# Performance work log

Measured on AMD Instinct MI355X. Metric: run time of the kernel, lower is better.

Reference implementation:

```python
import jax, jax.numpy as jnp
import numpy as np

B, L, D = 4, 8192, 1024
H, HD = 16, 64  # num_heads, head_dim (qkv_features = H*HD = 1024)
EPS = 1e-06


def elu_feature_map(x):
    return jax.nn.elu(x) + 1.0


def setup_inputs() -> dict:
    key = jax.random.key(0)
    ks = jax.random.split(key, 9)
    # xavier-uniform-ish scales
    def xav(k, shape, fan_in, fan_out):
        lim = jnp.sqrt(6.0 / (fan_in + fan_out))
        return jax.random.uniform(k, shape, jnp.float32, -lim, lim)
    x = jax.random.normal(ks[0], (B, L, D), jnp.float32)
    Wq = xav(ks[1], (D, H, HD), D, H * HD)
    Wk = xav(ks[2], (D, H, HD), D, H * HD)
    Wv = xav(ks[3], (D, H, HD), D, H * HD)
    Wo = xav(ks[4], (H, HD, D), H * HD, D)
    bq = jax.random.normal(ks[5], (H, HD), jnp.float32) * 1e-06
    bk = jax.random.normal(ks[6], (H, HD), jnp.float32) * 1e-06
    bv = jax.random.normal(ks[7], (H, HD), jnp.float32) * 1e-06
    bo = jax.random.normal(ks[8], (D,), jnp.float32) * 1e-06
    return {"x": x, "Wq": Wq, "bq": bq, "Wk": Wk, "bk": bk,
            "Wv": Wv, "bv": bv, "Wo": Wo, "bo": bo}


def reference(x, Wq, bq, Wk, bk, Wv, bv, Wo, bo):
    # QKV projections (DenseGeneral axis=-1 -> (H, HD))
    q = jnp.einsum('nld,dhk->nlhk', x, Wq) + bq  # [B,L,H,HD]
    k = jnp.einsum('nld,dhk->nlhk', x, Wk) + bk
    v = jnp.einsum('nld,dhk->nlhk', x, Wv) + bv
    # Kernelized linear attention
    qf = elu_feature_map(q)
    kf = elu_feature_map(k)
    kv = jnp.einsum('nshd,nshm->nhmd', kf, v)          # [B,H,HD,HD]
    z = 1.0 / (jnp.einsum('nlhd,nhd->nlh', qf, jnp.sum(kf, axis=1)) + EPS)
    y = jnp.einsum('nlhd,nhmd,nlh->nlhm', qf, kv, z)   # [B,L,H,HD]
    # Output projection (DenseGeneral over (-2,-1))
    out = jnp.einsum('nlhm,hmd->nld', y, Wo) + bo      # [B,L,D]
    return out
```

## Files before the change

### kernel.cpp

```cpp
#include <hip/hip_runtime.h>
#include <stdint.h>

typedef unsigned short u16;
typedef __attribute__((ext_vector_type(8))) short bf16x8;
typedef __attribute__((ext_vector_type(8))) unsigned short u16x8;
typedef __attribute__((ext_vector_type(4))) unsigned short u16x4;
typedef __attribute__((ext_vector_type(4))) float f32x4;

#define AS1 __attribute__((address_space(1)))
#define AS3 __attribute__((address_space(3)))

__device__ __forceinline__ u16 f32_to_bf16(float f) {
  unsigned int u = __builtin_bit_cast(unsigned int, f);
  u += 0x7FFFu + ((u >> 16) & 1u);
  return (u16)(u >> 16);
}
__device__ __forceinline__ float bf16_to_f32(u16 s) {
  return __builtin_bit_cast(float, (unsigned int)s << 16);
}
__device__ __forceinline__ void g2lds16(const void* g, void* l) {
  __builtin_amdgcn_global_load_lds((const AS1 void*)g, (AS3 void*)l, 16, 0, 0);
}

__global__ __launch_bounds__(256) void cvt_x(const float* __restrict__ x, u16* __restrict__ xb) {
  size_t base = ((size_t)blockIdx.x * 256 + threadIdx.x) * 8;
  const size_t stride = (size_t)2048 * 256 * 8;
  #pragma unroll
  for (int it = 0; it < 8; ++it, base += stride) {
    float4 a = *(const float4*)(x + base);
    float4 b = *(const float4*)(x + base + 4);
    u16x8 o;
    o[0]=f32_to_bf16(a.x); o[1]=f32_to_bf16(a.y); o[2]=f32_to_bf16(a.z); o[3]=f32_to_bf16(a.w);
    o[4]=f32_to_bf16(b.x); o[5]=f32_to_bf16(b.y); o[6]=f32_to_bf16(b.z); o[7]=f32_to_bf16(b.w);
    *(u16x8*)(xb + base) = o;
  }
}

__global__ void cvt_wt(const float* __restrict__ Wq, const float* __restrict__ Wk,
                       const float* __restrict__ Wv, const float* __restrict__ Wo,
                       u16* __restrict__ WT) {
  __shared__ float tile[32][33];
  const float* W = blockIdx.z==0 ? Wq : blockIdx.z==1 ? Wk : blockIdx.z==2 ? Wv : Wo;
  int n0 = blockIdx.x*32, k0 = blockIdx.y*32;
  int tx = threadIdx.x, ty = threadIdx.y;
  for (int r = ty; r < 32; r += 8)
    tile[r][tx] = W[(size_t)(k0+r)*1024 + n0 + tx];
  __syncthreads();
  u16* out = WT + (size_t)blockIdx.z*1024*1024;
  for (int r = ty; r < 32; r += 8)
    out[(size_t)(n0+r)*1024 + k0 + tx] = f32_to_bf16(tile[tx][r]);
}

__global__ __launch_bounds__(256) void init_vvT(u16* __restrict__ vvT) {
  int idx = blockIdx.x*256 + threadIdx.x;
  int p = idx >> 14, rem = idx & 16383;
  int row = 64 + (rem >> 10), col8 = (rem & 1023) * 8;
  u16 v = (row == 64) ? (u16)0x3F80 : (u16)0;
  u16x8 o = {v,v,v,v,v,v,v,v};
  *(u16x8*)(vvT + ((size_t)p*80 + row)*8192 + col8) = o;
}

template<int MODE>
__global__ __launch_bounds__(512) void gemm8(const u16* __restrict__ A, const u16* __restrict__ WT,
    const float* __restrict__ bq, const float* __restrict__ bk, const float* __restrict__ bv,
    u16* __restrict__ qf, u16* __restrict__ kfT, u16* __restrict__ vvT,
    float* __restrict__ fout) {
  extern __shared__ u16 lds[];
  const int z = (MODE==0) ? blockIdx.y : 3;
  const u16* Bt = WT + (size_t)z*1048576;
  int bid = blockIdx.x;
  int swz = (bid & 7)*64 + (bid >> 3);
  int rb = swz >> 2, cb = swz & 3;
  const int gm0 = rb*256, gn0 = cb*256;
  const int t = threadIdx.x, w = t>>6, l = t&63;
  const int wm = w>>2, wn = w&3;
  const int lrow = l & 15, lks = l >> 4;
  const int csw = (l&7) ^ (l>>3);
  const u16* aBase = A  + (size_t)(gm0 + w*8 + (l>>3))*1024 + csw*8;
  const u16* bBase = Bt + (size_t)(gn0 + w*8 + (l>>3))*1024 + csw*8;

  f32x4 acc[2][2][4][2];
  const f32x4 vzero = {0.f,0.f,0.f,0.f};
  #pragma unroll
  for (int a0=0;a0<2;++a0)
    #pragma unroll
    for (int b0i=0;b0i<2;++b0i)
      #pragma unroll
      for (int c0=0;c0<4;++c0)
        #pragma unroll
        for (int d0=0;d0<2;++d0) acc[a0][b0i][c0][d0] = vzero;

  #pragma unroll
  for (int half=0; half<2; ++half)
    #pragma unroll
    for (int j=0;j<2;++j) {
      g2lds16(aBase + (half*128 + j*64)*1024, (char*)lds + half*16384 + j*8192 + w*1024);
      g2lds16(bBase + (half*128 + j*64)*1024, (char*)lds + 65536 + half*16384 + j*8192 + w*1024);
    }
  asm volatile("s_waitcnt vmcnt(0)" ::: "memory");
  __builtin_amdgcn_s_barrier();
  asm volatile("" ::: "memory");

  for (int kt = 0; kt < 16; ++kt) {
    const int buf = kt & 1;
    const char* Ab = (const char*)lds + buf*32768;
    const char* Bb = (const char*)lds + 65536 + buf*32768;
    char* An = (char*)lds + (buf^1)*32768;
    char* Bn = (char*)lds + 65536 + (buf^1)*32768;
    const u16* aSrc = aBase + (size_t)(kt+1)*64;
    const u16* bSrc = bBase + (size_t)(kt+1)*64;
    const bool pf = (kt < 15);

    bf16x8 af0[4][2], af1[4][2];
    bf16x8 b0[2][2], b1[2][2];

    #define LD_A(DST,MH)                                                     \
      _Pragma("unroll")                                                      \
      for (int mi=0;mi<4;++mi) {                                             \
        int row = (MH)*128 + wm*64 + mi*16 + lrow;                           \
        _Pragma("unroll")                                                    \
        for (int kx=0;kx<2;++kx)                                             \
          DST[mi][kx] = *(const bf16x8*)(Ab + row*128 + (((kx*4+lks) ^ (row&7))<<4)); \
      }
    #define LD_B(DST,NH)                                                     \
      _Pragma("unroll")                                                      \
      for (int ni=0;ni<2;++ni) {                                             \
        int row = (NH)*128 + wn*32 + ni*16 + lrow;                           \
        _Pragma("unroll")                                                    \
        for (int kx=0;kx<2;++kx)                                             \
          DST[ni][kx] = *(const bf16x8*)(Bb + row*128 + (((kx*4+lks) ^ (row&7))<<4)); \
      }
    #define MFMA16(MH,NH,AF,BF)                                              \
      __builtin_amdgcn_s_setprio(1);                                         \
      _Pragma("unroll")                                                      \
      for (int mi=0;mi<4;++mi)                                               \
        _Pragma("unroll")                                                    \
        for (int ni=0;ni<2;++ni) {                                           \
          acc[MH][NH][mi][ni] = __builtin_amdgcn_mfma_f32_16x16x32_bf16(AF[mi][0], BF[ni][0], acc[MH][NH][mi][ni], 0,0,0); \
          acc[MH][NH][mi][ni] = __builtin_amdgcn_mfma_f32_16x16x32_bf16(AF[mi][1], BF[ni][1], acc[MH][NH][mi][ni], 0,0,0); \
        }                                                                    \
      __builtin_amdgcn_s_setprio(0);                                         \
      __builtin_amdgcn_s_barrier();                                          \
      asm volatile("" ::: "memory");

    LD_A(af0, 0); LD_B(b0, 0);
    if (pf) { g2lds16(aSrc, An + w*1024); g2lds16(aSrc + 64*1024, An + 8192 + w*1024); }
    if (pf) { asm volatile("s_waitcnt vmcnt(4)" ::: "memory"); }
    else    { asm volatile("s_waitcnt vmcnt(2)" ::: "memory"); }
    __builtin_amdgcn_s_barrier();
    asm volatile("" ::: "memory");
    LD_B(b1, 1);
    MFMA16(0, 0, af0, b0);

    if (pf) { g2lds16(bSrc, Bn + w*1024); g2lds16(bSrc + 64*1024, Bn + 8192 + w*1024); }
    if (pf) { asm volatile("s_waitcnt vmcnt(4)" ::: "memory"); }
    else    { asm volatile("s_waitcnt vmcnt(0)" ::: "memory"); }
    __builtin_amdgcn_s_barrier();
    asm volatile("" ::: "memory");
    LD_A(af1, 1);
    MFMA16(0, 1, af0, b1);

    if (pf) { g2lds16(bSrc + 128*1024, Bn + 16384 + w*1024); g2lds16(bSrc + 192*1024, Bn + 24576 + w*1024); }
    __builtin_amdgcn_s_barrier();
    asm volatile("" ::: "memory");
    MFMA16(1, 1, af1, b1);

    if (pf) { g2lds16(aSrc + 128*1024, An + 16384 + w*1024); g2lds16(aSrc + 192*1024, An + 24576 + w*1024); }
    if (pf) { asm volatile("s_waitcnt vmcnt(4)" ::: "memory"); }
    __builtin_amdgcn_s_barrier();
    asm volatile("" ::: "memory");
    MFMA16(1, 0, af1, b0);

    #undef LD_A
    #undef LD_B
    #undef MFMA16
  }

  if (MODE == 0) {
    const float* bias = z==0 ? bq : (z==1 ? bk : bv);
    const bool feat = (z < 2);
    if (z == 0) {
      #pragma unroll
      for (int mh=0;mh<2;++mh)
        #pragma unroll
        for (int nh=0;nh<2;++nh)
          #pragma unroll
          for (int mi=0;mi<4;++mi)
            #pragma unroll
            for (int ni=0;ni<2;++ni) {
              int n = gn0 + nh*128 + wn*32 + ni*16 + lrow;
              float bn = bias[n];
              int h = n>>6, hd = n&63;
              int mbase = gm0 + mh*128 + wm*64 + mi*16 + (lks<<2);
              #pragma unroll
              for (int r=0;r<4;++r) {
                int m = mbase + r;
                float val = acc[mh][nh][mi][ni][r] + bn;
                val = val>0.f ? val+1.f : __expf(val);
                qf[((size_t)((m>>13)*16 + h)*8192 + (m&8191))*64 + hd] = f32_to_bf16(val);
              }
            }
    } else {
      u16* outp = (z==1) ? kfT : vvT;
      const size_t prow = (z==1) ? 64 : 80;
      #pragma unroll
      for (int mh=0;mh<2;++mh)
        #pragma unroll
        for (int nh=0;nh<2;++nh)
          #pragma unroll
          for (int mi=0;mi<4;++mi)
            #pragma unroll
            for (int ni=0;ni<2;++ni) {
              int n = gn0 + nh*128 + wn*32 + ni*16 + lrow;
              float bn = bias[n];
              int h = n>>6, hd = n&63;
              int mbase = gm0 + mh*128 + wm*64 + mi*16 + (lks<<2);
              int b_ = mbase >> 13, s = mbase & 8191;
              u16x4 pk;
              #pragma unroll
              for (int r=0;r<4;++r) {
                float val = acc[mh][nh][mi][ni][r] + bn;
                if (feat) val = val>0.f ? val+1.f : __expf(val);
                pk[r] = f32_to_bf16(val);
              }
              *(u16x4*)(outp + ((size_t)(b_*16 + h)*prow + hd)*8192 + s) = pk;
            }
    }
  } else {
    #pragma unroll
    for (int mh=0;mh<2;++mh)
      #pragma unroll
      for (int nh=0;nh<2;++nh)
        #pragma unroll
        for (int mi=0;mi<4;++mi)
          #pragma unroll
          for (int ni=0;ni<2;++ni) {
            int n = gn0 + nh*128 + wn*32 + ni*16 + lrow;
            float bn = bq[n];
            int mbase = gm0 + mh*128 + wm*64 + mi*16 + (lks<<2);
            #pragma unroll
            for (int r=0;r<4;++r) {
              int m = mbase + r;
              fout[(size_t)m*1024 + n] = acc[mh][nh][mi][ni][r] + bn;
            }
          }
  }
}

__global__ __launch_bounds__(256) void kv_mfma(const u16* __restrict__ kfT, const u16* __restrict__ vvT,
                                               float* __restrict__ pkv) {
  __shared__ __align__(16) u16 lA[80*256];
  __shared__ __align__(16) u16 lB[64*256];
  const int p = blockIdx.x, c = blockIdx.y;
  const int t = threadIdx.x, w = t>>6, l = t&63;
  const int srow = t >> 5;
  const int csw = (t&31) ^ ((t>>5)&7);
  const u16* aRow = vvT + ((size_t)p*80 + srow)*8192 + (size_t)c*512 + csw*8;
  const u16* bRow = kfT + ((size_t)p*64 + srow)*8192 + (size_t)c*512 + csw*8;

  f32x4 acc5[5];
  const f32x4 vzero = {0.f,0.f,0.f,0.f};
  #pragma unroll
  for (int mi=0;mi<5;++mi) acc5[mi] = vzero;

  for (int sub = 0; sub < 2; ++sub) {
    const size_t so = (size_t)sub*256;
    #pragma unroll
    for (int i=0;i<10;++i)
      g2lds16(aRow + (size_t)i*8*8192 + so, (char*)lA + i*4096 + t*16);
    #pragma unroll
    for (int i=0;i<8;++i)
      g2lds16(bRow + (size_t)i*8*8192 + so, (char*)lB + i*4096 + t*16);
    asm volatile("s_waitcnt vmcnt(0)" ::: "memory");
    __builtin_amdgcn_s_barrier();
    asm volatile("" ::: "memory");
    #pragma unroll
    for (int ks=0;ks<8;++ks) {
      const int brow = w*16 + (l&15);
      const int slot = ks*4 + (l>>4);
      bf16x8 bfr = *(const bf16x8*)((const char*)lB + brow*512 + ((slot ^ (brow&7))<<4));
      #pragma unroll
      for (int mi=0;mi<5;++mi) {
        const int arow = mi*16 + (l&15);
        bf16x8 afr = *(const bf16x8*)((const char*)lA + arow*512 + ((slot ^ (arow&7))<<4));
        acc5[mi] = __builtin_amdgcn_mfma_f32_16x16x32_bf16(afr, bfr, acc5[mi], 0,0,0);
      }
    }
    __builtin_amdgcn_s_barrier();
    asm volatile("" ::: "memory");
  }

  float* po = pkv + ((size_t)p*16 + c)*5120;
  #pragma unroll
  for (int mi=0;mi<5;++mi)
    #pragma unroll
    for (int r=0;r<4;++r)
      po[(mi*16 + (l>>4)*4 + r)*64 + w*16 + (l&15)] = acc5[mi][r];
}

__global__ __launch_bounds__(256) void kv_reduce(const float* __restrict__ pkv, u16* __restrict__ bkv) {
  int p = blockIdx.x, t = threadIdx.x;
  for (int i = t; i < 5120; i += 256) {
    float s = 0.f;
    for (int c = 0; c < 16; ++c) s += pkv[((size_t)p*16 + c)*5120 + i];
    bkv[(size_t)p*5120 + i] = f32_to_bf16(s);
  }
}

__global__ __launch_bounds__(256) void y_gemm(const u16* __restrict__ qf, const u16* __restrict__ bkv,
                                              u16* __restrict__ y) {
  __shared__ __align__(16) u16 As[256*64];
  __shared__ __align__(16) u16 Bs[80*64];
  int p = blockIdx.x, rb = blockIdx.y;
  int t = threadIdx.x, wave = t >> 6, lane = t & 63;
  const u16* aslab = qf + ((size_t)p*8192 + (size_t)rb*256)*64;
  for (int i = t*8; i < 5120; i += 2048)
    *(int4*)&Bs[i] = *(const int4*)&bkv[(size_t)p*5120 + i];
  #pragma unroll
  for (int it = 0; it < 8; ++it)
    g2lds16(aslab + it*2048 + t*8, (char*)As + it*4096 + wave*1024);
  __syncthreads();
  const f32x4 vzero = {0.f,0.f,0.f,0.f};
  f32x4 acc[4][5];
  #pragma unroll
  for (int mi=0;mi<4;++mi)
    #pragma unroll
    for (int ni=0;ni<5;++ni) acc[mi][ni] = vzero;
  #pragma unroll
  for (int kk = 0; kk < 64; kk += 32) {
    bf16x8 af[4], bfr[5];
    #pragma unroll
    for (int mi=0;mi<4;++mi)
      af[mi] = *(const bf16x8*)&As[(wave*64 + mi*16 + (lane&15))*64 + kk + (lane>>4)*8];
    #pragma unroll
    for (int ni=0;ni<5;++ni)
      bfr[ni] = *(const bf16x8*)&Bs[(ni*16 + (lane&15))*64 + kk + (lane>>4)*8];
    #pragma unroll
    for (int mi=0;mi<4;++mi)
      #pragma unroll
      for (int ni=0;ni<5;++ni)
        acc[mi][ni] = __builtin_amdgcn_mfma_f32_16x16x32_bf16(af[mi], bfr[ni], acc[mi][ni], 0, 0, 0);
  }
  int b_ = p >> 4, h = p & 15;
  #pragma unroll
  for (int mi=0;mi<4;++mi) {
    #pragma unroll
    for (int r=0;r<4;++r) {
      float den = __shfl(acc[mi][4][r], lane & 48);
      float zf = 1.0f / (den + 1e-6f);
      int lq = rb*256 + wave*64 + mi*16 + ((lane>>4)<<2) + r;
      size_t rowbase = ((size_t)(b_*8192 + lq)*16 + h)*64;
      #pragma unroll
      for (int ni=0;ni<4;++ni)
        y[rowbase + ni*16 + (lane&15)] = f32_to_bf16(acc[mi][ni][r] * zf);
    }
  }
}

extern "C" void kernel_launch(void* const* d_in, const int* in_sizes, int n_in,
                              void* d_out, int out_size, void* d_ws, size_t ws_size,
                              hipStream_t stream) {
  const float* x  = (const float*)d_in[0];
  const float* Wq = (const float*)d_in[1];
  const float* bq = (const float*)d_in[2];
  const float* Wk = (const float*)d_in[3];
  const float* bk = (const float*)d_in[4];
  const float* Wv = (const float*)d_in[5];
  const float* bv = (const float*)d_in[6];
  const float* Wo = (const float*)d_in[7];
  const float* bo = (const float*)d_in[8];
  float* out = (float*)d_out;
  char* ws = (char*)d_ws;

  u16*  xb  = (u16*)(ws);
  u16*  WT  = (u16*)(ws + 67108864);
  u16*  qf  = (u16*)(ws + 75497472);
  u16*  kfT = (u16*)(ws + 142606336);
  u16*  vvT = (u16*)(ws + 209715200);
  u16*  bkv = (u16*)(ws + 293601280);
  float* pkv = (float*)(ws);
  u16*  yb  = xb;

  auto kq = gemm8<0>; auto ko = gemm8<1>;
  hipFuncSetAttribute((const void*)kq, hipFuncAttributeMaxDynamicSharedMemorySize, 131072);
  hipFuncSetAttribute((const void*)ko, hipFuncAttributeMaxDynamicSharedMemorySize, 131072);

  cvt_x<<<2048, 256, 0, stream>>>(x, xb);
  cvt_wt<<<dim3(32,32,4), dim3(32,8), 0, stream>>>(Wq, Wk, Wv, Wo, WT);
  init_vvT<<<4096, 256, 0, stream>>>(vvT);
  gemm8<0><<<dim3(512,3), 512, 131072, stream>>>(xb, WT, bq, bk, bv, qf, kfT, vvT, nullptr);
  kv_mfma<<<dim3(64,16), 256, 0, stream>>>(kfT, vvT, pkv);
  kv_reduce<<<64, 256, 0, stream>>>(pkv, bkv);
  y_gemm<<<dim3(64,32), 256, 0, stream>>>(qf, bkv, yb);
  gemm8<1><<<dim3(512,1), 512, 131072, stream>>>(yb, WT, bo, nullptr, nullptr, nullptr, nullptr, nullptr, out);
}
```

Baseline: 418.2 us.

## Restructure GEMM main loop into two 32-MFMA phases with merged prefetch

The GEMM inner loop goes from four 16-MFMA phases, each separated by a barrier, to two 32-MFMA phases. Both A fragments are loaded up front, and all four A prefetches and all four B prefetches are issued together. This halves the number of workgroup barriers per K-step and lengthens the MFMA runs between synchronisation points. In exchange it needs more live registers (both A fragment sets at once) and changes the vmcnt wait accounting, which could hurt overlap or occupancy.

```diff
diff --git a/kernel.cpp b/kernel.cpp
--- a/kernel.cpp
+++ b/kernel.cpp
@@ -130,50 +130,55 @@
         for (int kx=0;kx<2;++kx)                                             \
           DST[ni][kx] = *(const bf16x8*)(Bb + row*128 + (((kx*4+lks) ^ (row&7))<<4)); \
       }
-    #define MFMA16(MH,NH,AF,BF)                                              \
+    #define MFMA32(NH,BF)                                                    \
       __builtin_amdgcn_s_setprio(1);                                         \
       _Pragma("unroll")                                                      \
       for (int mi=0;mi<4;++mi)                                               \
         _Pragma("unroll")                                                    \
         for (int ni=0;ni<2;++ni) {                                           \
-          acc[MH][NH][mi][ni] = __builtin_amdgcn_mfma_f32_16x16x32_bf16(AF[mi][0], BF[ni][0], acc[MH][NH][mi][ni], 0,0,0); \
-          acc[MH][NH][mi][ni] = __builtin_amdgcn_mfma_f32_16x16x32_bf16(AF[mi][1], BF[ni][1], acc[MH][NH][mi][ni], 0,0,0); \
+          acc[0][NH][mi][ni] = __builtin_amdgcn_mfma_f32_16x16x32_bf16(af0[mi][0], BF[ni][0], acc[0][NH][mi][ni], 0,0,0); \
+          acc[0][NH][mi][ni] = __builtin_amdgcn_mfma_f32_16x16x32_bf16(af0[mi][1], BF[ni][1], acc[0][NH][mi][ni], 0,0,0); \
+        }                                                                    \
+      _Pragma("unroll")                                                      \
+      for (int mi=0;mi<4;++mi)                                               \
+        _Pragma("unroll")                                                    \
+        for (int ni=0;ni<2;++ni) {                                           \
+          acc[1][NH][mi][ni] = __builtin_amdgcn_mfma_f32_16x16x32_bf16(af1[mi][0], BF[ni][0], acc[1][NH][mi][ni], 0,0,0); \
+          acc[1][NH][mi][ni] = __builtin_amdgcn_mfma_f32_16x16x32_bf16(af1[mi][1], BF[ni][1], acc[1][NH][mi][ni], 0,0,0); \
         }                                                                    \
       __builtin_amdgcn_s_setprio(0);                                         \
       __builtin_amdgcn_s_barrier();                                          \
       asm volatile("" ::: "memory");
 
-    LD_A(af0, 0); LD_B(b0, 0);
-    if (pf) { g2lds16(aSrc, An + w*1024); g2lds16(aSrc + 64*1024, An + 8192 + w*1024); }
-    if (pf) { asm volatile("s_waitcnt vmcnt(4)" ::: "memory"); }
-    else    { asm volatile("s_waitcnt vmcnt(2)" ::: "memory"); }
+    LD_A(af0, 0); LD_A(af1, 1); LD_B(b0, 0);
+    if (pf) {
+      g2lds16(aSrc,            An + w*1024);
+      g2lds16(aSrc +  64*1024, An +  8192 + w*1024);
+      g2lds16(aSrc + 128*1024, An + 16384 + w*1024);
+      g2lds16(aSrc + 192*1024, An + 24576 + w*1024);
+      asm volatile("s_waitcnt vmcnt(4)" ::: "memory");
+    } else {
+      asm volatile("s_waitcnt vmcnt(0)" ::: "memory");
+    }
     __builtin_amdgcn_s_barrier();
     asm volatile("" ::: "memory");
     LD_B(b1, 1);
-    MFMA16(0, 0, af0, b0);
-
-    if (pf) { g2lds16(bSrc, Bn + w*1024); g2lds16(bSrc + 64*1024, Bn + 8192 + w*1024); }
-    if (pf) { asm volatile("s_waitcnt vmcnt(4)" ::: "memory"); }
-    else    { asm volatile("s_waitcnt vmcnt(0)" ::: "memory"); }
+    MFMA32(0, b0);
+
+    if (pf) {
+      g2lds16(bSrc,            Bn + w*1024);
+      g2lds16(bSrc +  64*1024, Bn +  8192 + w*1024);
+      g2lds16(bSrc + 128*1024, Bn + 16384 + w*1024);
+      g2lds16(bSrc + 192*1024, Bn + 24576 + w*1024);
+      asm volatile("s_waitcnt vmcnt(2)" ::: "memory");
+    }
     __builtin_amdgcn_s_barrier();
     asm volatile("" ::: "memory");
-    LD_A(af1, 1);
-    MFMA16(0, 1, af0, b1);
-
-    if (pf) { g2lds16(bSrc + 128*1024, Bn + 16384 + w*1024); g2lds16(bSrc + 192*1024, Bn + 24576 + w*1024); }
-    __builtin_amdgcn_s_barrier();
-    asm volatile("" ::: "memory");
-    MFMA16(1, 1, af1, b1);
-
-    if (pf) { g2lds16(aSrc + 128*1024, An + 16384 + w*1024); g2lds16(aSrc + 192*1024, An + 24576 + w*1024); }
-    if (pf) { asm volatile("s_waitcnt vmcnt(4)" ::: "memory"); }
-    __builtin_amdgcn_s_barrier();
-    asm volatile("" ::: "memory");
-    MFMA16(1, 0, af1, b0);
+    MFMA32(1, b1);
 
     #undef LD_A
     #undef LD_B
-    #undef MFMA16
+    #undef MFMA32
   }
 
   if (MODE == 0) {
```

Measured after the change: 465.3 us. 1.11x slower.
